# Optimization experiments

Measured on AMD Instinct MI355X. Metric: run time of the kernel, lower is better.

Reference implementation:

```python
import jax, jax.numpy as jnp
import numpy as np

N_NODES = 50000
N_EDGES = 650000
NEG_SLOPE = 0.2


def gat_conv(x, src, dst, W, a_src, a_dst, bias, concat):
    """PyG-style GATConv (eval mode, self-loops already included in src/dst).
    x: [N, F_in], W: [F_in, H*C], a_src/a_dst: [H, C], bias: [H*C] or [C]."""
    N = x.shape[0]
    H, C = a_src.shape
    h = (x @ W).reshape(N, H, C)                      # [N, H, C]
    al_src = (h * a_src).sum(-1)                      # [N, H]
    al_dst = (h * a_dst).sum(-1)                      # [N, H]
    logits = jax.nn.leaky_relu(al_src[src] + al_dst[dst], NEG_SLOPE)  # [E, H]
    # segment softmax over destination neighborhoods
    m = jax.ops.segment_max(logits, dst, num_segments=N)
    m = jnp.where(jnp.isfinite(m), m, 0.0)
    e = jnp.exp(logits - m[dst])
    s = jax.ops.segment_sum(e, dst, num_segments=N)
    alpha = e / (s[dst] + 1e-16)                      # [E, H]
    msg = alpha[:, :, None] * h[src]                  # [E, H, C]
    out = jax.ops.segment_sum(msg, dst, num_segments=N)  # [N, H, C]
    out = out.reshape(N, H * C) if concat else out.mean(axis=1)
    return out + bias


def setup_inputs() -> dict:
    key = jax.random.key(0)
    ks = jax.random.split(key, 16)
    IN, HID, H, OUT = 128, 64, 4, 1
    x = jax.random.normal(ks[0], (N_NODES, IN), dtype=jnp.float32)
    edge_index = jax.random.randint(ks[1], (2, N_EDGES), 0, N_NODES, dtype=jnp.int64)
    s = 0.1
    params = {
        'W1': jax.random.normal(ks[2], (IN, H * HID), dtype=jnp.float32) * s,
        'a_src1': jax.random.normal(ks[3], (H, HID), dtype=jnp.float32) * s,
        'a_dst1': jax.random.normal(ks[4], (H, HID), dtype=jnp.float32) * s,
        'b1': jnp.zeros((H * HID,), dtype=jnp.float32),
        'W2': jax.random.normal(ks[5], (H * HID, H * HID), dtype=jnp.float32) * s,
        'a_src2': jax.random.normal(ks[6], (H, HID), dtype=jnp.float32) * s,
        'a_dst2': jax.random.normal(ks[7], (H, HID), dtype=jnp.float32) * s,
        'b2': jnp.zeros((H * HID,), dtype=jnp.float32),
        'W3': jax.random.normal(ks[8], (H * HID, OUT), dtype=jnp.float32) * s,
        'a_src3': jax.random.normal(ks[9], (1, OUT), dtype=jnp.float32) * s,
        'a_dst3': jax.random.normal(ks[10], (1, OUT), dtype=jnp.float32) * s,
        'b3': jnp.zeros((OUT,), dtype=jnp.float32),
    }
    return {'x': x, 'edge_index': edge_index, **params}


def reference(x, edge_index, W1, a_src1, a_dst1, b1, W2, a_src2, a_dst2, b2, W3, a_src3, a_dst3, b3):
    N = x.shape[0]
    loops = jnp.arange(N, dtype=edge_index.dtype)
    src = jnp.concatenate([edge_index[0], loops])
    dst = jnp.concatenate([edge_index[1], loops])
    h = gat_conv(x, src, dst, W1, a_src1, a_dst1, b1, concat=True)
    h = jax.nn.elu(h)  # dropout: identity in eval mode
    h = gat_conv(h, src, dst, W2, a_src2, a_dst2, b2, concat=True)
    h = jax.nn.elu(h)
    out = gat_conv(h, src, dst, W3, a_src3, a_dst3, b3, concat=False)
    return out
```

## Files before the change

### kernel.cpp

```cpp
#include <hip/hip_runtime.h>
#include <math.h>

#define NN 50000
#define NE 650000
#define NET 700000
#define FD 256
#define NEG 0.2f

static __device__ __forceinline__ float lrelu(float v){ return v > 0.f ? v : NEG*v; }

static __device__ __forceinline__ unsigned short f2bf(float f){
  union { float f; unsigned u; } v; v.f = f;
  unsigned r = v.u + 0x7fff + ((v.u >> 16) & 1);
  return (unsigned short)(r >> 16);
}
static __device__ __forceinline__ float bf2f(unsigned short h){
  union { unsigned u; float f; } v; v.u = ((unsigned)h) << 16;
  return v.f;
}
static __device__ __forceinline__ float bflo(unsigned u){ return __uint_as_float(u << 16); }
static __device__ __forceinline__ float bfhi(unsigned u){ return __uint_as_float(u & 0xffff0000u); }

static __device__ __forceinline__ void gload_lds16(const unsigned short* g, unsigned short* l){
  __builtin_amdgcn_global_load_lds(
      (const __attribute__((address_space(1))) unsigned int*)(g),
      (__attribute__((address_space(3))) unsigned int*)(l), 16, 0, 0);
}

typedef __attribute__((ext_vector_type(8))) short short8_t;
typedef __attribute__((ext_vector_type(4))) float f32x4;

__global__ void count_deg(const int* __restrict__ ei, int* __restrict__ deg){
  int e = blockIdx.x*blockDim.x + threadIdx.x;
  if (e >= NET) return;
  int d = (e < NE) ? ei[NE + e] : (e - NE);
  atomicAdd(&deg[d], 1);
}

__global__ void scan_block(const int* __restrict__ deg, int* __restrict__ excl, int* __restrict__ bsums){
  __shared__ int sh[256];
  int t = threadIdx.x;
  int i0 = blockIdx.x*1024 + t*4;
  int v0 = (i0+0 < NN) ? deg[i0+0] : 0;
  int v1 = (i0+1 < NN) ? deg[i0+1] : 0;
  int v2 = (i0+2 < NN) ? deg[i0+2] : 0;
  int v3 = (i0+3 < NN) ? deg[i0+3] : 0;
  int tot = v0+v1+v2+v3;
  sh[t] = tot;
  __syncthreads();
  for (int off=1; off<256; off<<=1){
    int x = (t>=off) ? sh[t-off] : 0;
    __syncthreads();
    sh[t] += x;
    __syncthreads();
  }
  int base = sh[t] - tot;
  if (i0+0 < NN) excl[i0+0] = base;
  if (i0+1 < NN) excl[i0+1] = base + v0;
  if (i0+2 < NN) excl[i0+2] = base + v0+v1;
  if (i0+3 < NN) excl[i0+3] = base + v0+v1+v2;
  if (t == 255) bsums[blockIdx.x] = sh[255];
}

__global__ void scan_tops(int* bsums, int nb){
  if (threadIdx.x==0 && blockIdx.x==0){
    int run=0;
    for (int i=0;i<nb;i++){ int x=bsums[i]; bsums[i]=run; run+=x; }
  }
}

__global__ void scan_add(int* __restrict__ indptr, const int* __restrict__ bsums, int* __restrict__ cursor){
  int i = blockIdx.x*blockDim.x + threadIdx.x;
  if (i < NN){
    int v = indptr[i] + bsums[i>>10];
    indptr[i] = v;
    cursor[i] = v;
  }
  if (i == 0) indptr[NN] = NET;
}

__global__ void scatter_csr(const int* __restrict__ ei, int* __restrict__ cursor, int* __restrict__ csr){
  int e = blockIdx.x*blockDim.x + threadIdx.x;
  if (e >= NET) return;
  int s, d;
  if (e < NE){ s = ei[e]; d = ei[NE+e]; } else { s = e-NE; d = e-NE; }
  int pos = atomicAdd(&cursor[d], 1);
  csr[pos] = s;
}

__global__ void castBt(const float* __restrict__ B, unsigned short* __restrict__ bth,
                       unsigned short* __restrict__ btl, int K){
  int idx = blockIdx.x*blockDim.x + threadIdx.x;
  if (idx >= K*256) return;
  int k = idx >> 8, n = idx & 255;
  float f = B[idx];
  unsigned short h = f2bf(f);
  float lo = f - bf2f(h);
  bth[n*K + k] = h;
  btl[n*K + k] = f2bf(lo);
}

__global__ void castA(const float* __restrict__ x, unsigned short* __restrict__ xh,
                      unsigned short* __restrict__ xl, int n){
  int i = (blockIdx.x*blockDim.x + threadIdx.x)*4;
  if (i >= n) return;
  float4 f = *(const float4*)(x + i);
  ushort4 h, l;
  h.x = f2bf(f.x); l.x = f2bf(f.x - bf2f(h.x));
  h.y = f2bf(f.y); l.y = f2bf(f.y - bf2f(h.y));
  h.z = f2bf(f.z); l.z = f2bf(f.z - bf2f(h.z));
  h.w = f2bf(f.w); l.w = f2bf(f.w - bf2f(h.w));
  *(ushort4*)(xh + i) = h;
  *(ushort4*)(xl + i) = l;
}

__global__ __launch_bounds__(256, 2) void gemm_mfma(const unsigned short* __restrict__ Ahg,
                                                    const unsigned short* __restrict__ Alg,
                                                    const unsigned short* __restrict__ Bth,
                                                    const unsigned short* __restrict__ Btl,
                                                    unsigned short* __restrict__ Cb,
                                                    const float* __restrict__ a_src,
                                                    const float* __restrict__ a_dst,
                                                    float* __restrict__ al,
                                                    int M, int K){
  __shared__ unsigned short Ah[128*32], Al[128*32], Bh[128*32], Bl[128*32];
  int t = threadIdx.x;
  int wave = t >> 6, lane = t & 63;
  int wm = wave >> 1, wn = wave & 1;
  int quad = lane >> 4, l16 = lane & 15;
  int bm0 = blockIdx.y*128, bn0 = blockIdx.x*128;

  const unsigned short* gsrc = (wave==0)?Ahg:(wave==1)?Alg:(wave==2)?Bth:Btl;
  unsigned short* lbuf       = (wave==0)?Ah :(wave==1)?Al :(wave==2)?Bh :Bl;
  int sbase = (wave < 2) ? bm0 : bn0;
  int srow = lane >> 2;
  int skg  = (lane & 3) * 8;

  f32x4 acc[4][4];
  #pragma unroll
  for (int i=0;i<4;i++)
    #pragma unroll
    for (int j=0;j<4;j++) acc[i][j] = (f32x4){0.f,0.f,0.f,0.f};

  for (int k0 = 0; k0 < K; k0 += 32){
    __syncthreads();
    #pragma unroll
    for (int i=0;i<8;i++){
      int r = sbase + i*16 + srow;
      if (wave < 2) r = min(r, M-1);
      gload_lds16(gsrc + (size_t)r*K + k0 + skg, lbuf + i*512);
    }
    __syncthreads();

    short8_t afh[4], afl[4], bfh[4], bfl[4];
    #pragma unroll
    for (int mt=0; mt<4; ++mt){
      int row = wm*64 + mt*16 + l16;
      afh[mt] = *(short8_t*)&Ah[row*32 + quad*8];
      afl[mt] = *(short8_t*)&Al[row*32 + quad*8];
    }
    #pragma unroll
    for (int nt=0; nt<4; ++nt){
      int col = wn*64 + nt*16 + l16;
      bfh[nt] = *(short8_t*)&Bh[col*32 + quad*8];
      bfl[nt] = *(short8_t*)&Bl[col*32 + quad*8];
    }
    #pragma unroll
    for (int mt=0; mt<4; ++mt)
      #pragma unroll
      for (int nt=0; nt<4; ++nt){
        acc[mt][nt] = __builtin_amdgcn_mfma_f32_16x16x32_bf16(afh[mt], bfh[nt], acc[mt][nt], 0,0,0);
        acc[mt][nt] = __builtin_amdgcn_mfma_f32_16x16x32_bf16(afh[mt], bfl[nt], acc[mt][nt], 0,0,0);
        acc[mt][nt] = __builtin_amdgcn_mfma_f32_16x16x32_bf16(afl[mt], bfh[nt], acc[mt][nt], 0,0,0);
      }
  }

  __syncthreads();

  int head_w = (bn0 >> 6) + wn;
  float cs[4], cd[4];
  #pragma unroll
  for (int nt=0; nt<4; ++nt){
    cs[nt] = a_src[head_w*64 + nt*16 + l16];
    cd[nt] = a_dst[head_w*64 + nt*16 + l16];
  }
  {
    float* fsc = (float*)lbuf;
    int grow = bm0 + wm*64 + lane;
    #pragma unroll
    for (int pass=0; pass<2; ++pass){
      #pragma unroll
      for (int mt=0; mt<4; ++mt)
        #pragma unroll
        for (int r=0; r<4; ++r){
          float p = 0.f;
          #pragma unroll
          for (int nt=0; nt<4; ++nt)
            p += acc[mt][nt][r] * (pass ? cd[nt] : cs[nt]);
          fsc[(mt*16 + quad*4 + r)*17 + l16] = p;
        }
      float s = 0.f;
      #pragma unroll
      for (int j=0; j<16; ++j) s += fsc[lane*17 + j];
      if (grow < M) al[grow*8 + pass*4 + head_w] = s;
    }
  }

  unsigned short* tile = lbuf;
  #pragma unroll
  for (int mt=0; mt<4; ++mt)
    #pragma unroll
    for (int r=0; r<4; ++r){
      int rl = mt*16 + quad*4 + r;
      #pragma unroll
      for (int nt=0; nt<4; ++nt)
        tile[rl*64 + nt*16 + l16] = f2bf(acc[mt][nt][r]);
    }
  int orow = lane >> 3, ocol = (lane & 7) * 8;
  #pragma unroll
  for (int it=0; it<8; ++it){
    int rl = it*8 + orow;
    int row = bm0 + wm*64 + rl;
    if (row < M){
      uint4 v = *(uint4*)&tile[rl*64 + ocol];
      *(uint4*)(Cb + (size_t)row*FD + bn0 + wn*64 + ocol) = v;
    }
  }
}

static __device__ __forceinline__ void gather_chunk(int cnt, const float* eb, const int* sb,
                                                    const char* hp, int half, int head8,
                                                    float acc[8]){
  for (int tt = 0; tt < cnt; tt += 8){
    int e0 = tt + half, e1 = e0 + 2, e2 = e0 + 4, e3 = e0 + 6;
    int o0 = sb[e0], o1 = sb[e1], o2 = sb[e2], o3 = sb[e3];
    float v0 = eb[e0*4 + head8], v1 = eb[e1*4 + head8];
    float v2 = eb[e2*4 + head8], v3 = eb[e3*4 + head8];
    uint4 a = *(const uint4*)(hp + o0);
    uint4 b = *(const uint4*)(hp + o1);
    uint4 c = *(const uint4*)(hp + o2);
    uint4 d = *(const uint4*)(hp + o3);
    acc[0]+=v0*bflo(a.x); acc[1]+=v0*bfhi(a.x); acc[2]+=v0*bflo(a.y); acc[3]+=v0*bfhi(a.y);
    acc[4]+=v0*bflo(a.z); acc[5]+=v0*bfhi(a.z); acc[6]+=v0*bflo(a.w); acc[7]+=v0*bfhi(a.w);
    acc[0]+=v1*bflo(b.x); acc[1]+=v1*bfhi(b.x); acc[2]+=v1*bflo(b.y); acc[3]+=v1*bfhi(b.y);
    acc[4]+=v1*bflo(b.z); acc[5]+=v1*bfhi(b.z); acc[6]+=v1*bflo(b.w); acc[7]+=v1*bfhi(b.w);
    acc[0]+=v2*bflo(c.x); acc[1]+=v2*bfhi(c.x); acc[2]+=v2*bflo(c.y); acc[3]+=v2*bfhi(c.y);
    acc[4]+=v2*bflo(c.z); acc[5]+=v2*bfhi(c.z); acc[6]+=v2*bflo(c.w); acc[7]+=v2*bfhi(c.w);
    acc[0]+=v3*bflo(d.x); acc[1]+=v3*bfhi(d.x); acc[2]+=v3*bflo(d.y); acc[3]+=v3*bfhi(d.y);
    acc[4]+=v3*bflo(d.z); acc[5]+=v3*bfhi(d.z); acc[6]+=v3*bflo(d.w); acc[7]+=v3*bfhi(d.w);
  }
}

template<bool FUSE_W3>
__global__ __launch_bounds__(256) void gat_agg(const unsigned short* __restrict__ hb,
                                               const float* __restrict__ al,
                                               const int* __restrict__ indptr, const int* __restrict__ csr,
                                               const float* __restrict__ bias,
                                               unsigned short* __restrict__ outh,
                                               unsigned short* __restrict__ outl,
                                               const float* __restrict__ W3,
                                               float* __restrict__ h3){
  __shared__ float ebuf[4][256];
  __shared__ int   sbuf[4][64];
  int wv = threadIdx.x >> 6, lane = threadIdx.x & 63;
  int n = blockIdx.x*4 + wv;
  if (n >= NN) return;
  int half = lane >> 5, l32 = lane & 31, head8 = l32 >> 3;
  int base = indptr[n], deg = indptr[n+1] - base;
  float4 ald = *(const float4*)(al + n*8 + 4);
  float* eb = &ebuf[wv][0];
  int*   sb = &sbuf[wv][0];
  const char* hp = (const char*)hb + l32*16;

  float acc[8] = {0.f,0.f,0.f,0.f,0.f,0.f,0.f,0.f};
  float4 esum = make_float4(0.f,0.f,0.f,0.f);

  if (deg <= 64){
    int sj = 0;
    float4 lg = make_float4(-1e30f,-1e30f,-1e30f,-1e30f);
    if (lane < deg){
      sj = csr[base + lane];
      float4 als = *(const float4*)(al + sj*8);
      lg.x = lrelu(als.x + ald.x);
      lg.y = lrelu(als.y + ald.y);
      lg.z = lrelu(als.z + ald.z);
      lg.w = lrelu(als.w + ald.w);
    }
    float4 mx = lg;
    for (int off=32; off; off>>=1){
      mx.x = fmaxf(mx.x, __shfl_xor(mx.x, off));
      mx.y = fmaxf(mx.y, __shfl_xor(mx.y, off));
      mx.z = fmaxf(mx.z, __shfl_xor(mx.z, off));
      mx.w = fmaxf(mx.w, __shfl_xor(mx.w, off));
    }
    float4 e4 = make_float4(0.f,0.f,0.f,0.f);
    if (lane < deg){
      e4.x = expf(lg.x - mx.x); e4.y = expf(lg.y - mx.y);
      e4.z = expf(lg.z - mx.z); e4.w = expf(lg.w - mx.w);
    }
    esum = e4;
    *(float4*)&eb[lane*4] = e4;
    sb[lane] = sj << 9;
    gather_chunk(deg, eb, sb, hp, half, head8, acc);
  } else {
    float4 mx = make_float4(-1e30f,-1e30f,-1e30f,-1e30f);
    for (int j = lane; j < deg; j += 64){
      int s = csr[base+j];
      float4 als = *(const float4*)(al + s*8);
      mx.x = fmaxf(mx.x, lrelu(als.x + ald.x));
      mx.y = fmaxf(mx.y, lrelu(als.y + ald.y));
      mx.z = fmaxf(mx.z, lrelu(als.z + ald.z));
      mx.w = fmaxf(mx.w, lrelu(als.w + ald.w));
    }
    for (int off=32; off; off>>=1){
      mx.x = fmaxf(mx.x, __shfl_xor(mx.x, off));
      mx.y = fmaxf(mx.y, __shfl_xor(mx.y, off));
      mx.z = fmaxf(mx.z, __shfl_xor(mx.z, off));
      mx.w = fmaxf(mx.w, __shfl_xor(mx.w, off));
    }
    for (int j0 = 0; j0 < deg; j0 += 64){
      int j = j0 + lane;
      float4 e4 = make_float4(0.f,0.f,0.f,0.f);
      int sj = 0;
      if (j < deg){
        sj = csr[base+j];
        float4 als = *(const float4*)(al + sj*8);
        e4.x = expf(lrelu(als.x + ald.x) - mx.x);
        e4.y = expf(lrelu(als.y + ald.y) - mx.y);
        e4.z = expf(lrelu(als.z + ald.z) - mx.z);
        e4.w = expf(lrelu(als.w + ald.w) - mx.w);
        esum.x += e4.x; esum.y += e4.y; esum.z += e4.z; esum.w += e4.w;
      }
      *(float4*)&eb[lane*4] = e4;
      sb[lane] = sj << 9;
      gather_chunk(min(64, deg - j0), eb, sb, hp, half, head8, acc);
    }
  }

  for (int off=32; off; off>>=1){
    esum.x += __shfl_xor(esum.x, off);
    esum.y += __shfl_xor(esum.y, off);
    esum.z += __shfl_xor(esum.z, off);
    esum.w += __shfl_xor(esum.w, off);
  }
  #pragma unroll
  for (int i=0;i<8;i++) acc[i] += __shfl_xor(acc[i], 32);

  float sH = (head8==0)?esum.x:(head8==1)?esum.y:(head8==2)?esum.z:esum.w;
  float inv = 1.f/(sH + 1e-16f);
  int ch0 = l32*8;
  float4 b0 = *(const float4*)(bias + ch0);
  float4 b1 = *(const float4*)(bias + ch0 + 4);
  float o[8];
  o[0]=acc[0]*inv+b0.x; o[1]=acc[1]*inv+b0.y; o[2]=acc[2]*inv+b0.z; o[3]=acc[3]*inv+b0.w;
  o[4]=acc[4]*inv+b1.x; o[5]=acc[5]*inv+b1.y; o[6]=acc[6]*inv+b1.z; o[7]=acc[7]*inv+b1.w;
  #pragma unroll
  for (int i=0;i<8;i++) o[i] = o[i] > 0.f ? o[i] : expm1f(o[i]);

  if (FUSE_W3){
    float4 w0 = *(const float4*)(W3 + ch0);
    float4 w1 = *(const float4*)(W3 + ch0 + 4);
    float p = o[0]*w0.x + o[1]*w0.y + o[2]*w0.z + o[3]*w0.w
            + o[4]*w1.x + o[5]*w1.y + o[6]*w1.z + o[7]*w1.w;
    #pragma unroll
    for (int off=16; off; off>>=1) p += __shfl_xor(p, off);
    if (lane == 0) h3[n] = p;
  } else if (half == 0){
    unsigned hi[4], lo[4];
    #pragma unroll
    for (int i=0;i<4;i++){
      unsigned short h0 = f2bf(o[2*i]),   h1 = f2bf(o[2*i+1]);
      unsigned short g0 = f2bf(o[2*i]   - bf2f(h0));
      unsigned short g1 = f2bf(o[2*i+1] - bf2f(h1));
      hi[i] = (unsigned)h0 | ((unsigned)h1 << 16);
      lo[i] = (unsigned)g0 | ((unsigned)g1 << 16);
    }
    *(uint4*)(outh + (size_t)n*FD + ch0) = make_uint4(hi[0],hi[1],hi[2],hi[3]);
    *(uint4*)(outl + (size_t)n*FD + ch0) = make_uint4(lo[0],lo[1],lo[2],lo[3]);
  }
}

__global__ __launch_bounds__(256) void gat_agg3(const float* __restrict__ h3, const int* __restrict__ indptr,
                                                const int* __restrict__ csr, const float* __restrict__ asrc,
                                                const float* __restrict__ adst, const float* __restrict__ b3,
                                                float* __restrict__ out){
  int n = blockIdx.x*blockDim.x + threadIdx.x;
  if (n >= NN) return;
  float as = asrc[0], ad = adst[0];
  float hd = h3[n]*ad;
  int base = indptr[n], end = indptr[n+1];
  float m = -1e30f;
  for (int e=base; e<end; ++e){
    float l = lrelu(as*h3[csr[e]] + hd);
    m = fmaxf(m, l);
  }
  float s = 0.f, w = 0.f;
  for (int e=base; e<end; ++e){
    float hv = h3[csr[e]];
    float l = lrelu(as*hv + hd);
    float ee = expf(l - m);
    s += ee; w += ee*hv;
  }
  out[n] = w/(s + 1e-16f) + b3[0];
}

extern "C" void kernel_launch(void* const* d_in, const int* in_sizes, int n_in,
                              void* d_out, int out_size, void* d_ws, size_t ws_size,
                              hipStream_t stream){
  const float* x   = (const float*)d_in[0];
  const int*   ei  = (const int*)d_in[1];
  const float* W1  = (const float*)d_in[2];
  const float* as1 = (const float*)d_in[3];
  const float* ad1 = (const float*)d_in[4];
  const float* b1  = (const float*)d_in[5];
  const float* W2  = (const float*)d_in[6];
  const float* as2 = (const float*)d_in[7];
  const float* ad2 = (const float*)d_in[8];
  const float* b2  = (const float*)d_in[9];
  const float* W3  = (const float*)d_in[10];
  const float* as3 = (const float*)d_in[11];
  const float* ad3 = (const float*)d_in[12];
  const float* b3  = (const float*)d_in[13];
  float* outp = (float*)d_out;

  char* w = (char*)d_ws;
  size_t off = 0;
  auto alloc = [&](size_t bytes)->void*{
    void* p = w + off; off += (bytes + 255) & ~(size_t)255; return p;
  };
  unsigned short* hb  = (unsigned short*)alloc((size_t)NN*FD*2);
  unsigned short* oh  = (unsigned short*)alloc((size_t)NN*FD*2);
  unsigned short* ol  = (unsigned short*)alloc((size_t)NN*FD*2);
  unsigned short* xh  = (unsigned short*)alloc((size_t)NN*128*2);
  unsigned short* xl  = (unsigned short*)alloc((size_t)NN*128*2);
  float* al    = (float*)alloc((size_t)NN*8*4);
  int*   indptr= (int*)alloc((size_t)(NN+1)*4);
  int*   cursor= (int*)alloc((size_t)NN*4);
  int*   csr   = (int*)alloc((size_t)NET*4);
  int*   bsums = (int*)alloc(64*4);
  float* h3    = (float*)alloc((size_t)NN*4);
  unsigned short* bt1h = (unsigned short*)alloc((size_t)256*128*2);
  unsigned short* bt1l = (unsigned short*)alloc((size_t)256*128*2);
  unsigned short* bt2h = (unsigned short*)alloc((size_t)256*256*2);
  unsigned short* bt2l = (unsigned short*)alloc((size_t)256*256*2);

  hipMemsetAsync(cursor, 0, (size_t)NN*4, stream);
  count_deg<<<(NET+255)/256, 256, 0, stream>>>(ei, cursor);
  int nb = (NN+1023)/1024;
  scan_block<<<nb, 256, 0, stream>>>(cursor, indptr, bsums);
  scan_tops<<<1, 64, 0, stream>>>(bsums, nb);
  scan_add<<<(NN+255)/256, 256, 0, stream>>>(indptr, bsums, cursor);
  scatter_csr<<<(NET+255)/256, 256, 0, stream>>>(ei, cursor, csr);

  castBt<<<128, 256, 0, stream>>>(W1, bt1h, bt1l, 128);
  castBt<<<256, 256, 0, stream>>>(W2, bt2h, bt2l, 256);
  castA<<<(NN*128/4+255)/256, 256, 0, stream>>>(x, xh, xl, NN*128);

  dim3 gemm_grid(FD/128, (NN+127)/128);
  int agg_blocks = (NN+3)/4;

  gemm_mfma<<<gemm_grid, 256, 0, stream>>>(xh, xl, bt1h, bt1l, hb, as1, ad1, al, NN, 128);
  gat_agg<false><<<agg_blocks, 256, 0, stream>>>(hb, al, indptr, csr, b1, oh, ol, nullptr, nullptr);
  gemm_mfma<<<gemm_grid, 256, 0, stream>>>(oh, ol, bt2h, bt2l, hb, as2, ad2, al, NN, 256);
  gat_agg<true><<<agg_blocks, 256, 0, stream>>>(hb, al, indptr, csr, b2, nullptr, nullptr, W3, h3);
  gat_agg3<<<(NN+255)/256, 256, 0, stream>>>(h3, indptr, csr, as3, ad3, b3, outp);
}
```

Before: 379.1 us.

## Assign one node per half-wave in GAT aggregation and drop softmax max pass

The aggregation kernel now maps each destination node to 32 lanes instead of a full 64-lane wave, so each block handles 8 nodes. This suits the small average degree and removes the cross-half accumulator shuffle. It also drops the max-subtraction pass of the segment softmax and uses fast __expf, which saves one gather pass over neighbour logits. The trade-offs are possible exp overflow for large logits and divergence between the two halves of a wave when neighbouring nodes have different degrees.

```diff
diff --git a/kernel.cpp b/kernel.cpp
--- a/kernel.cpp
+++ b/kernel.cpp
@@ -228,29 +228,6 @@
   }
 }
 
-static __device__ __forceinline__ void gather_chunk(int cnt, const float* eb, const int* sb,
-                                                    const char* hp, int half, int head8,
-                                                    float acc[8]){
-  for (int tt = 0; tt < cnt; tt += 8){
-    int e0 = tt + half, e1 = e0 + 2, e2 = e0 + 4, e3 = e0 + 6;
-    int o0 = sb[e0], o1 = sb[e1], o2 = sb[e2], o3 = sb[e3];
-    float v0 = eb[e0*4 + head8], v1 = eb[e1*4 + head8];
-    float v2 = eb[e2*4 + head8], v3 = eb[e3*4 + head8];
-    uint4 a = *(const uint4*)(hp + o0);
-    uint4 b = *(const uint4*)(hp + o1);
-    uint4 c = *(const uint4*)(hp + o2);
-    uint4 d = *(const uint4*)(hp + o3);
-    acc[0]+=v0*bflo(a.x); acc[1]+=v0*bfhi(a.x); acc[2]+=v0*bflo(a.y); acc[3]+=v0*bfhi(a.y);
-    acc[4]+=v0*bflo(a.z); acc[5]+=v0*bfhi(a.z); acc[6]+=v0*bflo(a.w); acc[7]+=v0*bfhi(a.w);
-    acc[0]+=v1*bflo(b.x); acc[1]+=v1*bfhi(b.x); acc[2]+=v1*bflo(b.y); acc[3]+=v1*bfhi(b.y);
-    acc[4]+=v1*bflo(b.z); acc[5]+=v1*bfhi(b.z); acc[6]+=v1*bflo(b.w); acc[7]+=v1*bfhi(b.w);
-    acc[0]+=v2*bflo(c.x); acc[1]+=v2*bfhi(c.x); acc[2]+=v2*bflo(c.y); acc[3]+=v2*bfhi(c.y);
-    acc[4]+=v2*bflo(c.z); acc[5]+=v2*bfhi(c.z); acc[6]+=v2*bflo(c.w); acc[7]+=v2*bfhi(c.w);
-    acc[0]+=v3*bflo(d.x); acc[1]+=v3*bfhi(d.x); acc[2]+=v3*bflo(d.y); acc[3]+=v3*bfhi(d.y);
-    acc[4]+=v3*bflo(d.z); acc[5]+=v3*bfhi(d.z); acc[6]+=v3*bflo(d.w); acc[7]+=v3*bfhi(d.w);
-  }
-}
-
 template<bool FUSE_W3>
 __global__ __launch_bounds__(256) void gat_agg(const unsigned short* __restrict__ hb,
                                                const float* __restrict__ al,
@@ -260,92 +237,65 @@
                                                unsigned short* __restrict__ outl,
                                                const float* __restrict__ W3,
                                                float* __restrict__ h3){
-  __shared__ float ebuf[4][256];
-  __shared__ int   sbuf[4][64];
-  int wv = threadIdx.x >> 6, lane = threadIdx.x & 63;
-  int n = blockIdx.x*4 + wv;
+  __shared__ float ebuf[8][128];
+  __shared__ int   sbuf[8][32];
+  int wave = threadIdx.x >> 6, lane = threadIdx.x & 63;
+  int half = lane >> 5, l32 = lane & 31;
+  int slot = wave*2 + half;
+  int n = blockIdx.x*8 + slot;
   if (n >= NN) return;
-  int half = lane >> 5, l32 = lane & 31, head8 = l32 >> 3;
+  int head8 = l32 >> 3;
   int base = indptr[n], deg = indptr[n+1] - base;
   float4 ald = *(const float4*)(al + n*8 + 4);
-  float* eb = &ebuf[wv][0];
-  int*   sb = &sbuf[wv][0];
+  float* eb = &ebuf[slot][0];
+  int*   sb = &sbuf[slot][0];
   const char* hp = (const char*)hb + l32*16;
 
   float acc[8] = {0.f,0.f,0.f,0.f,0.f,0.f,0.f,0.f};
   float4 esum = make_float4(0.f,0.f,0.f,0.f);
 
-  if (deg <= 64){
+  for (int j0 = 0; j0 < deg; j0 += 32){
+    int j = j0 + l32;
+    float4 e4 = make_float4(0.f,0.f,0.f,0.f);
     int sj = 0;
-    float4 lg = make_float4(-1e30f,-1e30f,-1e30f,-1e30f);
-    if (lane < deg){
-      sj = csr[base + lane];
+    if (j < deg){
+      sj = csr[base + j];
       float4 als = *(const float4*)(al + sj*8);
-      lg.x = lrelu(als.x + ald.x);
-      lg.y = lrelu(als.y + ald.y);
-      lg.z = lrelu(als.z + ald.z);
-      lg.w = lrelu(als.w + ald.w);
-    }
-    float4 mx = lg;
-    for (int off=32; off; off>>=1){
-      mx.x = fmaxf(mx.x, __shfl_xor(mx.x, off));
-      mx.y = fmaxf(mx.y, __shfl_xor(mx.y, off));
-      mx.z = fmaxf(mx.z, __shfl_xor(mx.z, off));
-      mx.w = fmaxf(mx.w, __shfl_xor(mx.w, off));
-    }
-    float4 e4 = make_float4(0.f,0.f,0.f,0.f);
-    if (lane < deg){
-      e4.x = expf(lg.x - mx.x); e4.y = expf(lg.y - mx.y);
-      e4.z = expf(lg.z - mx.z); e4.w = expf(lg.w - mx.w);
-    }
-    esum = e4;
-    *(float4*)&eb[lane*4] = e4;
-    sb[lane] = sj << 9;
-    gather_chunk(deg, eb, sb, hp, half, head8, acc);
-  } else {
-    float4 mx = make_float4(-1e30f,-1e30f,-1e30f,-1e30f);
-    for (int j = lane; j < deg; j += 64){
-      int s = csr[base+j];
-      float4 als = *(const float4*)(al + s*8);
-      mx.x = fmaxf(mx.x, lrelu(als.x + ald.x));
-      mx.y = fmaxf(mx.y, lrelu(als.y + ald.y));
-      mx.z = fmaxf(mx.z, lrelu(als.z + ald.z));
-      mx.w = fmaxf(mx.w, lrelu(als.w + ald.w));
-    }
-    for (int off=32; off; off>>=1){
-      mx.x = fmaxf(mx.x, __shfl_xor(mx.x, off));
-      mx.y = fmaxf(mx.y, __shfl_xor(mx.y, off));
-      mx.z = fmaxf(mx.z, __shfl_xor(mx.z, off));
-      mx.w = fmaxf(mx.w, __shfl_xor(mx.w, off));
-    }
-    for (int j0 = 0; j0 < deg; j0 += 64){
-      int j = j0 + lane;
-      float4 e4 = make_float4(0.f,0.f,0.f,0.f);
-      int sj = 0;
-      if (j < deg){
-        sj = csr[base+j];
-        float4 als = *(const float4*)(al + sj*8);
-        e4.x = expf(lrelu(als.x + ald.x) - mx.x);
-        e4.y = expf(lrelu(als.y + ald.y) - mx.y);
-        e4.z = expf(lrelu(als.z + ald.z) - mx.z);
-        e4.w = expf(lrelu(als.w + ald.w) - mx.w);
-        esum.x += e4.x; esum.y += e4.y; esum.z += e4.z; esum.w += e4.w;
-      }
-      *(float4*)&eb[lane*4] = e4;
-      sb[lane] = sj << 9;
-      gather_chunk(min(64, deg - j0), eb, sb, hp, half, head8, acc);
-    }
-  }
-
-  for (int off=32; off; off>>=1){
+      e4.x = __expf(lrelu(als.x + ald.x));
+      e4.y = __expf(lrelu(als.y + ald.y));
+      e4.z = __expf(lrelu(als.z + ald.z));
+      e4.w = __expf(lrelu(als.w + ald.w));
+      esum.x += e4.x; esum.y += e4.y; esum.z += e4.z; esum.w += e4.w;
+    }
+    *(float4*)&eb[l32*4] = e4;
+    sb[l32] = sj << 9;
+    int cnt  = min(32, deg - j0);
+    int cpad = (cnt + 3) & ~3;
+    for (int tt = 0; tt < cpad; tt += 4){
+      int o0 = sb[tt], o1 = sb[tt+1], o2 = sb[tt+2], o3 = sb[tt+3];
+      float v0 = eb[tt*4 + head8],     v1 = eb[(tt+1)*4 + head8];
+      float v2 = eb[(tt+2)*4 + head8], v3 = eb[(tt+3)*4 + head8];
+      uint4 a = *(const uint4*)(hp + o0);
+      uint4 b = *(const uint4*)(hp + o1);
+      uint4 c = *(const uint4*)(hp + o2);
+      uint4 d = *(const uint4*)(hp + o3);
+      acc[0]+=v0*bflo(a.x); acc[1]+=v0*bfhi(a.x); acc[2]+=v0*bflo(a.y); acc[3]+=v0*bfhi(a.y);
+      acc[4]+=v0*bflo(a.z); acc[5]+=v0*bfhi(a.z); acc[6]+=v0*bflo(a.w); acc[7]+=v0*bfhi(a.w);
+      acc[0]+=v1*bflo(b.x); acc[1]+=v1*bfhi(b.x); acc[2]+=v1*bflo(b.y); acc[3]+=v1*bfhi(b.y);
+      acc[4]+=v1*bflo(b.z); acc[5]+=v1*bfhi(b.z); acc[6]+=v1*bflo(b.w); acc[7]+=v1*bfhi(b.w);
+      acc[0]+=v2*bflo(c.x); acc[1]+=v2*bfhi(c.x); acc[2]+=v2*bflo(c.y); acc[3]+=v2*bfhi(c.y);
+      acc[4]+=v2*bflo(c.z); acc[5]+=v2*bfhi(c.z); acc[6]+=v2*bflo(c.w); acc[7]+=v2*bfhi(c.w);
+      acc[0]+=v3*bflo(d.x); acc[1]+=v3*bfhi(d.x); acc[2]+=v3*bflo(d.y); acc[3]+=v3*bfhi(d.y);
+      acc[4]+=v3*bflo(d.z); acc[5]+=v3*bfhi(d.z); acc[6]+=v3*bflo(d.w); acc[7]+=v3*bfhi(d.w);
+    }
+  }
+
+  for (int off=16; off; off>>=1){
     esum.x += __shfl_xor(esum.x, off);
     esum.y += __shfl_xor(esum.y, off);
     esum.z += __shfl_xor(esum.z, off);
     esum.w += __shfl_xor(esum.w, off);
   }
-  #pragma unroll
-  for (int i=0;i<8;i++) acc[i] += __shfl_xor(acc[i], 32);
-
   float sH = (head8==0)?esum.x:(head8==1)?esum.y:(head8==2)?esum.z:esum.w;
   float inv = 1.f/(sH + 1e-16f);
   int ch0 = l32*8;
@@ -364,8 +314,8 @@
             + o[4]*w1.x + o[5]*w1.y + o[6]*w1.z + o[7]*w1.w;
     #pragma unroll
     for (int off=16; off; off>>=1) p += __shfl_xor(p, off);
-    if (lane == 0) h3[n] = p;
-  } else if (half == 0){
+    if (l32 == 0) h3[n] = p;
+  } else {
     unsigned hi[4], lo[4];
     #pragma unroll
     for (int i=0;i<4;i++){
@@ -457,7 +407,7 @@
   castA<<<(NN*128/4+255)/256, 256, 0, stream>>>(x, xh, xl, NN*128);
 
   dim3 gemm_grid(FD/128, (NN+127)/128);
-  int agg_blocks = (NN+3)/4;
+  int agg_blocks = (NN+7)/8;
 
   gemm_mfma<<<gemm_grid, 256, 0, stream>>>(xh, xl, bt1h, bt1l, hb, as1, ad1, al, NN, 128);
   gat_agg<false><<<agg_blocks, 256, 0, stream>>>(hb, al, indptr, csr, b1, oh, ol, nullptr, nullptr);
```

After: 367.2 us. -3.1%, faster.
